# Optimization experiments

Hardware: AMD Instinct MI355X
Metric: run time of the kernel (lower is better)

Reference implementation:

```python
import jax, jax.numpy as jnp
import numpy as np

DK, DV, NH, KS, STRIDE = 256, 256, 8, 3, 1
PAD = (KS - 1) // 2


def conv1d(x, w, b, stride=1, pad=PAD):
    # x: (B, Cin, W), w: (Cout, Cin, K)
    y = jax.lax.conv_general_dilated(
        x, w, window_strides=(stride,), padding=[(pad, pad)],
        dimension_numbers=("NCH", "OIH", "NCH"))
    return y + b[None, :, None]


def setup_inputs() -> dict:
    key = jax.random.key(0)
    ks = jax.random.split(key, 7)
    B, C, W = 8, 256, 2048
    OUT = 512
    x = jax.random.normal(ks[0], (B, C, W), dtype=jnp.float32)
    w_conv = jax.random.normal(ks[1], (OUT - DV, C, KS), dtype=jnp.float32) * 0.05
    b_conv = jax.random.normal(ks[2], (OUT - DV,), dtype=jnp.float32) * 0.05
    w_qkv = jax.random.normal(ks[3], (2 * DK + DV, C, KS), dtype=jnp.float32) * 0.05
    b_qkv = jax.random.normal(ks[4], (2 * DK + DV,), dtype=jnp.float32) * 0.05
    w_attn = jax.random.normal(ks[5], (DV, DV), dtype=jnp.float32) * 0.05
    b_attn = jax.random.normal(ks[6], (DV,), dtype=jnp.float32) * 0.05
    return {"x": x, "w_conv": w_conv, "b_conv": b_conv,
            "w_qkv": w_qkv, "b_qkv": b_qkv,
            "w_attn": w_attn, "b_attn": b_attn}


def reference(x, w_conv, b_conv, w_qkv, b_qkv, w_attn, b_attn):
    B, _, _ = x.shape
    dkh, dvh = DK // NH, DV // NH

    conv_out = conv1d(x, w_conv, b_conv, stride=STRIDE)   # (B, out-dv, W)
    W_out = conv_out.shape[-1]

    qkv = conv1d(x, w_qkv, b_qkv, stride=STRIDE)          # (B, 2dk+dv, W)
    q, k, v = jnp.split(qkv, [DK, 2 * DK], axis=1)
    q = q.reshape(B, NH, dkh, W_out) * (dkh ** -0.5)      # flat_q
    k = k.reshape(B, NH, dkh, W_out)                      # flat_k
    v = v.reshape(B, NH, dvh, W_out)                      # flat_v

    # logits = flat_q^T @ flat_k : (B, NH, W, W)
    logits = jnp.einsum("bhdq,bhdk->bhqk", q, k)
    weights = jax.nn.softmax(logits, axis=-1)
    # attn = weights @ flat_v^T : (B, NH, W, dvh)
    attn = jnp.einsum("bhqk,bhdk->bhqd", weights, v)
    # NOTE: original torch code RESHAPES (B,NH,W,dvh)->(B,NH,dvh,1,W) (no transpose),
    # then combines heads to (B, NH*dvh, 1, W). Reproduce faithfully:
    attn = attn.reshape(B, DV, W_out)
    # 1x1 conv on attention output
    attn = jnp.einsum("oc,bcw->bow", w_attn, attn) + b_attn[None, :, None]

    return jnp.concatenate([conv_out, attn], axis=1)      # (B, out_channels, W)
```

## Files before the change

kernel.cpp:

```cpp
#include <hip/hip_runtime.h>

typedef _Float16 f16;
typedef _Float16 f16x8 __attribute__((ext_vector_type(8)));
typedef _Float16 f16x4 __attribute__((ext_vector_type(4)));
typedef _Float16 f16x2 __attribute__((ext_vector_type(2)));
typedef __fp16 fp16x2 __attribute__((ext_vector_type(2)));
typedef float f32x4 __attribute__((ext_vector_type(4)));

static __device__ __forceinline__ f32x4 mfma32(f16x8 a, f16x8 b, f32x4 c) {
  return __builtin_amdgcn_mfma_f32_16x16x32_f16(a, b, c, 0, 0, 0);
}
static __device__ __forceinline__ void gload16(const void* g, void* l) {
  __builtin_amdgcn_global_load_lds(
      (const __attribute__((address_space(1))) unsigned int*)g,
      (__attribute__((address_space(3))) unsigned int*)l, 16, 0, 0);
}
static __device__ __forceinline__ f16x2 exp2pk(float a, float b) {
  union { fp16x2 i; f16x2 o; } u;
  u.i = __builtin_amdgcn_cvt_pkrtz(__builtin_amdgcn_exp2f(a), __builtin_amdgcn_exp2f(b));
  return u.o;
}
static __device__ __forceinline__ f16x8 cat4(f16x2 a, f16x2 b, f16x2 c, f16x2 d) {
  union { f16x2 h2[4]; f16x8 h8; } u;
  u.h2[0] = a; u.h2[1] = b; u.h2[2] = c; u.h2[3] = d;
  return u.h8;
}
static __device__ __forceinline__ f16x8 cat44(f16x4 lo, f16x4 hi) {
  union { f16x4 h4[2]; f16x8 h8; } u;
  u.h4[0] = lo; u.h4[1] = hi;
  return u.h8;
}

#define QSCALE_L2 0.25503626336707584f
#define SH_L2  12.98425536800067f

#define OFF_XT   0
#define OFF_WP   8396800
#define OFF_WA   9969664
#define OFF_BIAS 10100736
#define OFF_Q    10104832
#define OFF_K    18493440
#define OFF_V    26882048
#define OFF_AT   35270656

__global__ void prep_x_kernel(const float* __restrict__ x, f16* __restrict__ xTc) {
  if (blockIdx.x == 4096) {
    for (int i = threadIdx.x; i < 4096; i += 256) {
      int b = i >> 9, r = (i >> 8) & 1, ck = (i >> 5) & 7, ci = i & 31;
      xTc[((size_t)(b * 8 + ck) * 2050 + (r ? 2049 : 0)) * 32 + ci] = (f16)0.f;
    }
    return;
  }
  int gid = blockIdx.x * 256 + threadIdx.x;
  int w4 = gid & 511;
  int c  = (gid >> 9) & 255;
  int b  = gid >> 17;
  const float4 v = *(const float4*)(x + ((size_t)(b * 256 + c) * 2048 + w4 * 4));
  f16* p = xTc + ((size_t)(b * 8 + (c >> 5)) * 2050 + 1 + w4 * 4) * 32 + (c & 31);
  p[0]  = (f16)v.x;
  p[32] = (f16)v.y;
  p[64] = (f16)v.z;
  p[96] = (f16)v.w;
}

__global__ void prep_w_kernel(const float* __restrict__ wc, const float* __restrict__ bc,
                              const float* __restrict__ wq, const float* __restrict__ bq,
                              const float* __restrict__ wa_in,
                              f16* __restrict__ wpc, f16* __restrict__ wa,
                              float* __restrict__ biasp) {
  const int bid = blockIdx.x, tid = threadIdx.x;
  if (bid < 3072) {
    const int n = bid & 1023, t = bid >> 10, c = tid;
    float v;
    if (n < 256) {
      v = wc[(n * 256 + c) * 3 + t];
    } else {
      const int j = n - 256;
      v = wq[((size_t)j * 256 + c) * 3 + t];
      if (j < 256) v *= QSCALE_L2;
    }
    wpc[((size_t)(t * 8 + (c >> 5)) * 1024 + n) * 32 + (c & 31)] = (f16)v;
  } else if (bid < 3328) {
    const int o = bid - 3072;
    wa[o * 256 + tid] = (f16)wa_in[o * 256 + tid];
  } else {
    for (int n = tid; n < 1024; n += 256) {
      float v = (n < 256) ? bc[n] : ((n < 512) ? bq[n - 256] * QSCALE_L2 : bq[n - 256]);
      biasp[n] = v;
    }
  }
}

__global__ __launch_bounds__(256, 4) void conv_kernel(
    const f16* __restrict__ xTc, const f16* __restrict__ wpc,
    const float* __restrict__ biasp, float* __restrict__ out,
    f16* __restrict__ q_ws, f16* __restrict__ k_ws, f16* __restrict__ v_pk) {
  __shared__ __align__(16) char sm[32768];

  const int fid = blockIdx.x;
  const int b   = fid & 7;
  const int g   = fid >> 3;
  const int ocb = (g & 7) * 128;
  const int wb  = (g >> 3) * 128;
  const int tid = threadIdx.x;
  const int wid = tid >> 6, l = tid & 63, lr = l & 15, lg = l >> 4;
  const int wm = wid >> 1, wn = wid & 1;

  f32x4 acc[4][4];
#pragma unroll
  for (int i = 0; i < 4; ++i)
#pragma unroll
    for (int j = 0; j < 4; ++j) acc[i][j] = (f32x4){0.f, 0.f, 0.f, 0.f};

  const int swu = (tid >> 2) * 64 + (((tid & 3) ^ ((tid >> 3) & 3)) * 16);
  const char* agb = (const char*)xTc + (size_t)b * 1049600 + (size_t)wb * 64 + swu;
  const char* bgb = (const char*)wpc + (size_t)ocb * 64 + swu;
  char* al = sm + tid * 16;
  char* bl = sm + 16384 + tid * 16;

  const int sx  = ((lr >> 1) & 3) << 4;
  const int foa = (wm * 64 + lr) * 64 + ((lg * 16) ^ sx);
  const int fob = (wn * 64 + lr) * 64 + ((lg * 16) ^ sx);

  auto stage = [&](int s, int pb) {
    const int offA = (s & 7) * 131200 + (s >> 3) * 64;
    const int offB = s * 65536;
    gload16(agb + offA,        al + pb * 8192);
    gload16(agb + offA + 4096, al + pb * 8192 + 4096);
    gload16(bgb + offB,        bl + pb * 8192);
    gload16(bgb + offB + 4096, bl + pb * 8192 + 4096);
  };

  auto compute = [&](int pb) {
    const char* ab = sm + pb * 8192;
    const char* bb = sm + 16384 + pb * 8192;
    f16x8 af[4], bf[4];
#pragma unroll
    for (int mt = 0; mt < 4; ++mt) af[mt] = *(const f16x8*)(ab + foa + mt * 1024);
#pragma unroll
    for (int nt = 0; nt < 4; ++nt) bf[nt] = *(const f16x8*)(bb + fob + nt * 1024);
    __builtin_amdgcn_s_setprio(1);
#pragma unroll
    for (int mt = 0; mt < 4; ++mt)
#pragma unroll
      for (int nt = 0; nt < 4; ++nt)
        acc[mt][nt] = mfma32(af[mt], bf[nt], acc[mt][nt]);
    __builtin_amdgcn_s_setprio(0);
  };

#define VMW(n) asm volatile("s_waitcnt vmcnt(" #n ")" ::: "memory")
#define BAR()  __builtin_amdgcn_s_barrier()
#define SCB()  __builtin_amdgcn_sched_barrier(0)

  stage(0, 0);
#pragma unroll 1
  for (int s = 0; s < 23; ++s) {
    stage(s + 1, (s + 1) & 1);
    VMW(4); BAR(); SCB();
    compute(s & 1);
    BAR();
  }
  VMW(0); BAR(); SCB();
  compute(1);

#pragma unroll
  for (int nt = 0; nt < 4; ++nt) {
    const int oc = ocb + wn * 64 + nt * 16 + lr;
    const float bias = biasp[oc];
#pragma unroll
    for (int mt = 0; mt < 4; ++mt) {
      const int w0 = wb + wm * 64 + mt * 16 + lg * 4;
      const float v0 = acc[mt][nt][0] + bias;
      const float v1 = acc[mt][nt][1] + bias;
      const float v2 = acc[mt][nt][2] + bias;
      const float v3 = acc[mt][nt][3] + bias;
      if (oc < 256) {
        float4 o4 = {v0, v1, v2, v3};
        *(float4*)(out + (size_t)(b * 512 + oc) * 2048 + w0) = o4;
      } else if (oc < 768) {
        const int d  = oc - 256;
        f16* dst = (d < 256) ? q_ws : k_ws;
        const int dd = d & 31, h = (d >> 5) & 7;
        f16* p = dst + (size_t)((b * 8 + h) * 2048 + w0) * 32 + dd;
        p[0]  = (f16)v0;
        p[32] = (f16)v1;
        p[64] = (f16)v2;
        p[96] = (f16)v3;
      } else {
        const int d = oc - 768;
        const int dd = d & 31, h = d >> 5;
        f16x4 o4 = {(f16)v0, (f16)v1, (f16)v2, (f16)v3};
        *(f16x4*)(v_pk + (size_t)(b * 8 + h) * 65536 +
                  (w0 >> 6) * 2048 + ((w0 >> 4) & 3) * 512 + dd * 16 + (w0 & 15)) = o4;
      }
    }
  }
#undef VMW
#undef BAR
#undef SCB
}

__global__ __launch_bounds__(512, 4) void attn_kernel(
    const f16* __restrict__ q_ws, const f16* __restrict__ k_ws,
    const f16* __restrict__ v_pk, f16* __restrict__ aT) {
  __shared__ __align__(16) f16 Kl[2][2048];
  __shared__ __align__(16) f16 Vl[2][2048];

  const int fid = blockIdx.x;
  const int qb  = fid >> 6;
  const int bh  = ((fid & 7) << 3) | ((fid >> 3) & 7);
  const int tid = threadIdx.x, wid = tid >> 6, l = tid & 63, lr = l & 15, lg = l >> 4;
  const int b = bh >> 3, h = bh & 7;
  const size_t qk_base = (size_t)bh * 2048 * 32;

  const int u = tid & 255;
  const char* gp = (tid < 256)
      ? (const char*)(k_ws + qk_base) + (u >> 2) * 64 + ((u & 3) ^ ((u >> 3) & 3)) * 16
      : (const char*)(v_pk + (size_t)bh * 65536) + (u >> 1) * 32 + ((u & 1) ^ ((u >> 3) & 1)) * 16;
  char* lp = ((tid < 256) ? (char*)(&Kl[0][0]) : (char*)(&Vl[0][0])) + u * 16;

  const int qrow0 = qb * 256 + wid * 32;
  f16x8 qf0 = *(const f16x8*)(q_ws + qk_base + (size_t)(qrow0 + lr) * 32 + lg * 8);
  f16x8 qf1 = *(const f16x8*)(q_ws + qk_base + (size_t)(qrow0 + 16 + lr) * 32 + lg * 8);

  f32x4 accO[2][2];
  f32x4 ssum[2];
#pragma unroll
  for (int i = 0; i < 2; ++i) {
    ssum[i] = (f32x4){0.f, 0.f, 0.f, 0.f};
#pragma unroll
    for (int j = 0; j < 2; ++j) accO[i][j] = (f32x4){0.f, 0.f, 0.f, 0.f};
  }
  const f32x4 minit = {-SH_L2, -SH_L2, -SH_L2, -SH_L2};
  const f16x8 ones8 = {(f16)1.f, (f16)1.f, (f16)1.f, (f16)1.f,
                       (f16)1.f, (f16)1.f, (f16)1.f, (f16)1.f};

  const int kfo = lr * 64 + ((lg * 16) ^ (((lr >> 1) & 3) << 4));
  const int vfo = lr * 32 + (((lg >> 1) * 16) ^ (((lr >> 2) & 1) << 4)) + (lg & 1) * 8;

  auto stage = [&](int pb) {
    gload16(gp, lp + pb * 4096);
    gp += 4096;
  };

  auto compute = [&](int pb) {
    const char* kbuf = (const char*)(&Kl[0][0]) + pb * 4096;
    const char* vbuf = (const char*)(&Vl[0][0]) + pb * 4096;
    f32x4 s0[4], s1[4];
    __builtin_amdgcn_s_setprio(1);
#pragma unroll
    for (int mt = 0; mt < 4; ++mt) {
      f16x8 kf = *(const f16x8*)(kbuf + kfo + mt * 1024);
      s0[mt] = mfma32(kf, qf0, minit);
      s1[mt] = mfma32(kf, qf1, minit);
    }
    __builtin_amdgcn_s_setprio(0);
#pragma unroll
    for (int ks = 0; ks < 2; ++ks) {
      f16x8 pa0 = cat4(exp2pk(s0[2*ks][0], s0[2*ks][1]), exp2pk(s0[2*ks][2], s0[2*ks][3]),
                       exp2pk(s0[2*ks+1][0], s0[2*ks+1][1]), exp2pk(s0[2*ks+1][2], s0[2*ks+1][3]));
      f16x8 pa1 = cat4(exp2pk(s1[2*ks][0], s1[2*ks][1]), exp2pk(s1[2*ks][2], s1[2*ks][3]),
                       exp2pk(s1[2*ks+1][0], s1[2*ks+1][1]), exp2pk(s1[2*ks+1][2], s1[2*ks+1][3]));
      f16x8 vf0 = cat44(*(const f16x4*)(vbuf + vfo + (2*ks) * 1024),
                        *(const f16x4*)(vbuf + vfo + (2*ks+1) * 1024));
      f16x8 vf1 = cat44(*(const f16x4*)(vbuf + vfo + (2*ks) * 1024 + 512),
                        *(const f16x4*)(vbuf + vfo + (2*ks+1) * 1024 + 512));
      __builtin_amdgcn_s_setprio(1);
      accO[0][0] = mfma32(vf0, pa0, accO[0][0]);
      accO[0][1] = mfma32(vf0, pa1, accO[0][1]);
      accO[1][0] = mfma32(vf1, pa0, accO[1][0]);
      accO[1][1] = mfma32(vf1, pa1, accO[1][1]);
      ssum[0] = mfma32(ones8, pa0, ssum[0]);
      ssum[1] = mfma32(ones8, pa1, ssum[1]);
      __builtin_amdgcn_s_setprio(0);
    }
  };

#define VMW(n) asm volatile("s_waitcnt vmcnt(" #n ")" ::: "memory")
#define BAR()  __builtin_amdgcn_s_barrier()
#define SCB()  __builtin_amdgcn_sched_barrier(0)

  stage(0);
#pragma unroll 1
  for (int t = 0; t < 31; ++t) {
    stage((t + 1) & 1);
    VMW(1); BAR(); SCB();
    compute(t & 1);
    BAR();
  }
  VMW(0); BAR(); SCB();
  compute(1);

#pragma unroll
  for (int nt = 0; nt < 2; ++nt) {
    const float inv = 1.f / ssum[nt][0];
    const int q = qrow0 + nt * 16 + lr;
    const int cc = h * 32 + (q >> 6);
    const int wr = (q & 63) * 32;
#pragma unroll
    for (int dvt = 0; dvt < 2; ++dvt)
#pragma unroll
      for (int r = 0; r < 4; ++r) {
        const int dv = dvt * 16 + lg * 4 + r;
        aT[((size_t)b * 2048 + wr + dv) * 256 + cc] = (f16)(accO[dvt][nt][r] * inv);
      }
  }
#undef VMW
#undef BAR
#undef SCB
}

__global__ __launch_bounds__(256, 4) void proj_kernel(
    const f16* __restrict__ aT, const f16* __restrict__ wa,
    const float* __restrict__ b_attn, float* __restrict__ out) {
  const int fid = blockIdx.x;
  const int b  = fid & 7;
  const int g  = fid >> 3;
  const int ob = (g & 1) * 128;
  const int wb = (g >> 1) * 128;
  const int tid = threadIdx.x;
  const int wid = tid >> 6, l = tid & 63, lr = l & 15, lg = l >> 4;
  const int wm = wid >> 1, wn = wid & 1;

  f32x4 acc[4][4];
#pragma unroll
  for (int i = 0; i < 4; ++i)
#pragma unroll
    for (int j = 0; j < 4; ++j) acc[i][j] = (f32x4){0.f, 0.f, 0.f, 0.f};

  const f16* ab = aT + (size_t)(b * 2048 + wb + wm * 64 + lr) * 256 + lg * 8;
  const f16* wb_p = wa + (size_t)(ob + wn * 64 + lr) * 256 + lg * 8;

  for (int ks = 0; ks < 8; ++ks) {
    const int co = ks * 32;
    f16x8 af[4], bf[4];
#pragma unroll
    for (int mt = 0; mt < 4; ++mt) af[mt] = *(const f16x8*)(ab + (size_t)mt * 16 * 256 + co);
#pragma unroll
    for (int nt = 0; nt < 4; ++nt) bf[nt] = *(const f16x8*)(wb_p + (size_t)nt * 16 * 256 + co);
    __builtin_amdgcn_s_setprio(1);
#pragma unroll
    for (int mt = 0; mt < 4; ++mt)
#pragma unroll
      for (int nt = 0; nt < 4; ++nt) acc[mt][nt] = mfma32(af[mt], bf[nt], acc[mt][nt]);
    __builtin_amdgcn_s_setprio(0);
  }

#pragma unroll
  for (int nt = 0; nt < 4; ++nt) {
    const int o = ob + wn * 64 + nt * 16 + lr;
    const float bias = b_attn[o];
#pragma unroll
    for (int mt = 0; mt < 4; ++mt) {
      const int w0 = wb + wm * 64 + mt * 16 + lg * 4;
      float4 o4 = {acc[mt][nt][0] + bias, acc[mt][nt][1] + bias,
                   acc[mt][nt][2] + bias, acc[mt][nt][3] + bias};
      *(float4*)(out + (size_t)(b * 512 + 256 + o) * 2048 + w0) = o4;
    }
  }
}

extern "C" void kernel_launch(void* const* d_in, const int* in_sizes, int n_in,
                              void* d_out, int out_size, void* d_ws, size_t ws_size,
                              hipStream_t stream) {
  const float* x      = (const float*)d_in[0];
  const float* w_conv = (const float*)d_in[1];
  const float* b_conv = (const float*)d_in[2];
  const float* w_qkv  = (const float*)d_in[3];
  const float* b_qkv  = (const float*)d_in[4];
  const float* w_attn = (const float*)d_in[5];
  const float* b_attn = (const float*)d_in[6];
  float* out = (float*)d_out;

  char* ws = (char*)d_ws;
  f16*   xTc   = (f16*)(ws + OFF_XT);
  f16*   wpc   = (f16*)(ws + OFF_WP);
  f16*   wa    = (f16*)(ws + OFF_WA);
  float* biasp = (float*)(ws + OFF_BIAS);
  f16*   q_ws  = (f16*)(ws + OFF_Q);
  f16*   k_ws  = (f16*)(ws + OFF_K);
  f16*   v_pk  = (f16*)(ws + OFF_V);
  f16*   aT    = (f16*)(ws + OFF_AT);

  prep_x_kernel<<<4097, 256, 0, stream>>>(x, xTc);
  prep_w_kernel<<<3329, 256, 0, stream>>>(w_conv, b_conv, w_qkv, b_qkv, w_attn, wpc, wa, biasp);
  conv_kernel<<<1024, 256, 0, stream>>>(xTc, wpc, biasp, out, q_ws, k_ws, v_pk);
  attn_kernel<<<512, 512, 0, stream>>>(q_ws, k_ws, v_pk, aT);
  proj_kernel<<<256, 256, 0, stream>>>(aT, wa, b_attn, out);
}
```

Before: 141.6 us.

## Enlarge conv GEMM tile to 256x256 with 512 threads and 4-slot staging

The conv GEMM kernel moves from 128x128 tiles with 4 waves and a double buffer to 256x256 tiles with 8 waves. Each wave accumulates an 8x4 grid of 16x16 MFMA tiles, and loads are split into interleaved A and B half-phases over a 4-slot, 128KB LDS ring. The goal is more arithmetic intensity per global load and fewer blocks. The cost is one block per CU, only 256 blocks on a large-CU device (under one wave of work), higher register pressure, and less latency hiding.

```diff
diff --git a/kernel.cpp b/kernel.cpp
--- a/kernel.cpp
+++ b/kernel.cpp
@@ -91,60 +91,66 @@
   }
 }
 
-__global__ __launch_bounds__(256, 4) void conv_kernel(
+__global__ __launch_bounds__(512, 1) void conv_kernel(
     const f16* __restrict__ xTc, const f16* __restrict__ wpc,
     const float* __restrict__ biasp, float* __restrict__ out,
     f16* __restrict__ q_ws, f16* __restrict__ k_ws, f16* __restrict__ v_pk) {
-  __shared__ __align__(16) char sm[32768];
+  __shared__ __align__(16) char smA[65536];
+  __shared__ __align__(16) char smB[65536];
 
   const int fid = blockIdx.x;
   const int b   = fid & 7;
   const int g   = fid >> 3;
-  const int ocb = (g & 7) * 128;
-  const int wb  = (g >> 3) * 128;
+  const int ocb = (g & 3) * 256;
+  const int wb  = (g >> 2) * 256;
   const int tid = threadIdx.x;
   const int wid = tid >> 6, l = tid & 63, lr = l & 15, lg = l >> 4;
-  const int wm = wid >> 1, wn = wid & 1;
-
-  f32x4 acc[4][4];
-#pragma unroll
-  for (int i = 0; i < 4; ++i)
+  const int wm = wid >> 2, wn = wid & 3;
+
+  f32x4 acc[8][4];
+#pragma unroll
+  for (int i = 0; i < 8; ++i)
 #pragma unroll
     for (int j = 0; j < 4; ++j) acc[i][j] = (f32x4){0.f, 0.f, 0.f, 0.f};
 
   const int swu = (tid >> 2) * 64 + (((tid & 3) ^ ((tid >> 3) & 3)) * 16);
   const char* agb = (const char*)xTc + (size_t)b * 1049600 + (size_t)wb * 64 + swu;
   const char* bgb = (const char*)wpc + (size_t)ocb * 64 + swu;
-  char* al = sm + tid * 16;
-  char* bl = sm + 16384 + tid * 16;
-
-  const int sx  = ((lr >> 1) & 3) << 4;
-  const int foa = (wm * 64 + lr) * 64 + ((lg * 16) ^ sx);
-  const int fob = (wn * 64 + lr) * 64 + ((lg * 16) ^ sx);
-
-  auto stage = [&](int s, int pb) {
-    const int offA = (s & 7) * 131200 + (s >> 3) * 64;
-    const int offB = s * 65536;
-    gload16(agb + offA,        al + pb * 8192);
-    gload16(agb + offA + 4096, al + pb * 8192 + 4096);
-    gload16(bgb + offB,        bl + pb * 8192);
-    gload16(bgb + offB + 4096, bl + pb * 8192 + 4096);
+
+  const int sx   = ((lr >> 1) & 3) << 4;
+  const int foa0 = (wm * 128 + lr) * 64 + ((lg * 16) ^ sx);
+  const int fob0 = (wn * 64 + lr) * 64 + ((lg * 16) ^ sx);
+
+  auto stageA = [&](int kt, int kk) {
+    const int t = kt >> 2, ck = ((kt & 3) << 1) | kk;
+    const char* src = agb + (size_t)ck * 131200 + t * 64;
+    char* dst = smA + ((2 * kt + kk) & 3) * 16384 + tid * 16;
+    gload16(src, dst);
+    gload16(src + 8192, dst + 8192);
   };
-
-  auto compute = [&](int pb) {
-    const char* ab = sm + pb * 8192;
-    const char* bb = sm + 16384 + pb * 8192;
+  auto stageB = [&](int kt, int kk) {
+    const int t = kt >> 2, ck = ((kt & 3) << 1) | kk;
+    const char* src = bgb + (size_t)(t * 8 + ck) * 65536;
+    char* dst = smB + ((2 * kt + kk) & 3) * 16384 + tid * 16;
+    gload16(src, dst);
+    gload16(src + 8192, dst + 8192);
+  };
+
+  auto phase = [&](int kt, int mh, int kk) {
+    const int slot = (2 * kt + kk) & 3;
+    const char* ab = smA + slot * 16384;
+    const char* bb = smB + slot * 16384;
     f16x8 af[4], bf[4];
 #pragma unroll
-    for (int mt = 0; mt < 4; ++mt) af[mt] = *(const f16x8*)(ab + foa + mt * 1024);
-#pragma unroll
-    for (int nt = 0; nt < 4; ++nt) bf[nt] = *(const f16x8*)(bb + fob + nt * 1024);
+    for (int mt = 0; mt < 4; ++mt) af[mt] = *(const f16x8*)(ab + foa0 + mh * 4096 + mt * 1024);
+#pragma unroll
+    for (int nt = 0; nt < 4; ++nt) bf[nt] = *(const f16x8*)(bb + fob0 + nt * 1024);
     __builtin_amdgcn_s_setprio(1);
 #pragma unroll
     for (int mt = 0; mt < 4; ++mt)
 #pragma unroll
       for (int nt = 0; nt < 4; ++nt)
-        acc[mt][nt] = mfma32(af[mt], bf[nt], acc[mt][nt]);
+        acc[mh * 4 + mt][nt] = mfma32(af[mt], bf[nt], acc[mh * 4 + mt][nt]);
     __builtin_amdgcn_s_setprio(0);
   };
 
@@ -152,28 +158,35 @@
 #define BAR()  __builtin_amdgcn_s_barrier()
 #define SCB()  __builtin_amdgcn_sched_barrier(0)
 
-  stage(0, 0);
+  stageA(0, 0); stageB(0, 0); stageA(0, 1); stageB(0, 1);
+
 #pragma unroll 1
-  for (int s = 0; s < 23; ++s) {
-    stage(s + 1, (s + 1) & 1);
-    VMW(4); BAR(); SCB();
-    compute(s & 1);
-    BAR();
-  }
-  VMW(0); BAR(); SCB();
-  compute(1);
+  for (int kt = 0; kt < 11; ++kt) {
+    stageA(kt + 1, 0); VMW(6); BAR(); SCB(); phase(kt, 0, 0);
+    stageB(kt + 1, 0);         BAR(); SCB(); phase(kt, 1, 0);
+    stageA(kt + 1, 1); VMW(6); BAR(); SCB(); phase(kt, 0, 1);
+    stageB(kt + 1, 1);         BAR(); SCB(); phase(kt, 1, 1);
+  }
+  VMW(4); BAR(); SCB(); phase(11, 0, 0);
+          BAR(); SCB(); phase(11, 1, 0);
+  VMW(0); BAR(); SCB(); phase(11, 0, 1);
+          BAR(); SCB(); phase(11, 1, 1);
+
+#undef VMW
+#undef BAR
+#undef SCB
 
 #pragma unroll
   for (int nt = 0; nt < 4; ++nt) {
     const int oc = ocb + wn * 64 + nt * 16 + lr;
     const float bias = biasp[oc];
 #pragma unroll
-    for (int mt = 0; mt < 4; ++mt) {
-      const int w0 = wb + wm * 64 + mt * 16 + lg * 4;
-      const float v0 = acc[mt][nt][0] + bias;
-      const float v1 = acc[mt][nt][1] + bias;
-      const float v2 = acc[mt][nt][2] + bias;
-      const float v3 = acc[mt][nt][3] + bias;
+    for (int am = 0; am < 8; ++am) {
+      const int w0 = wb + wm * 128 + am * 16 + lg * 4;
+      const float v0 = acc[am][nt][0] + bias;
+      const float v1 = acc[am][nt][1] + bias;
+      const float v2 = acc[am][nt][2] + bias;
+      const float v3 = acc[am][nt][3] + bias;
       if (oc < 256) {
         float4 o4 = {v0, v1, v2, v3};
         *(float4*)(out + (size_t)(b * 512 + oc) * 2048 + w0) = o4;
@@ -195,9 +208,6 @@
       }
     }
   }
-#undef VMW
-#undef BAR
-#undef SCB
 }
 
 __global__ __launch_bounds__(512, 4) void attn_kernel(
@@ -384,7 +394,7 @@
 
   prep_x_kernel<<<4097, 256, 0, stream>>>(x, xTc);
   prep_w_kernel<<<3329, 256, 0, stream>>>(w_conv, b_conv, w_qkv, b_qkv, w_attn, wpc, wa, biasp);
-  conv_kernel<<<1024, 256, 0, stream>>>(xTc, wpc, biasp, out, q_ws, k_ws, v_pk);
+  conv_kernel<<<256, 512, 0, stream>>>(xTc, wpc, biasp, out, q_ws, k_ws, v_pk);
   attn_kernel<<<512, 512, 0, stream>>>(q_ws, k_ws, v_pk, aT);
   proj_kernel<<<256, 256, 0, stream>>>(aT, wa, b_attn, out);
 }
```

Measured after the change: 134.8 us. 4.8% less time.
